# Kernel optimization log

Hardware: AMD Instinct MI355X
Metric: run time of the kernel (lower is better)

Reference implementation:

```python
import jax, jax.numpy as jnp
import numpy as np

B, T, H, W = 8, 16, 512, 512


def setup_inputs() -> dict:
    key = jax.random.key(0)
    k1, k2 = jax.random.split(key)
    img = jax.random.normal(k1, (B, H, W), dtype=jnp.float32)
    U = jax.random.normal(k2, (B, T, H, W, 2), dtype=jnp.float32)
    return {"img": img, "U": U}


def _warp(img, U):
    # img: (B,H,W), U: (B,T,H,W,2) displacement (di, dj). Output (B,T,H,W).
    b, h, w = img.shape
    ii = jnp.arange(h, dtype=jnp.float32)[:, None]   # (H,1)
    jj = jnp.arange(w, dtype=jnp.float32)[None, :]   # (1,W)
    si = ii - U[..., 0]                              # (B,T,H,W) sample rows
    sj = jj - U[..., 1]                              # (B,T,H,W) sample cols
    i0 = jnp.clip(jnp.floor(si).astype(jnp.int32), 0, h - 1)
    j0 = jnp.clip(jnp.floor(sj).astype(jnp.int32), 0, w - 1)
    i1 = jnp.clip(i0 + 1, 0, h - 1)
    j1 = jnp.clip(j0 + 1, 0, w - 1)
    # fractional weights computed AFTER clipping, matching the original
    di = si - i0.astype(jnp.float32)
    dj = sj - j0.astype(jnp.float32)

    def gather(im, ri, ci):  # im (H,W), ri/ci (T,H,W)
        return im[ri, ci]

    g = jax.vmap(gather)  # over batch
    f00 = g(img, i0, j0)
    f01 = g(img, i0, j1)
    f10 = g(img, i1, j0)
    f11 = g(img, i1, j1)
    f0 = f00 + (f01 - f00) * dj
    f1 = f10 + (f11 - f10) * dj
    return f0 + (f1 - f0) * di


def reference(img, U):
    return _warp(img, U)
```

## Files before the change

kernel.cpp:

```cpp
#include <hip/hip_runtime.h>

#define HH 512
#define WW 512
#define TT 16
#define NROWS 16
#define SLOT_OFF 7

typedef float vf4 __attribute__((ext_vector_type(4)));
typedef float vf2 __attribute__((ext_vector_type(2)));

__device__ __forceinline__ float warp_one(const float* __restrict__ lds,
                                          const float* __restrict__ im,
                                          int ic, float fi, float fj,
                                          float ux, float uy) {
    float si = fi - ux;
    float sj = fj - uy;
    int i0 = (int)floorf(si);
    int j0 = (int)floorf(sj);
    i0 = min(max(i0, 0), HH - 1);
    j0 = min(max(j0, 0), WW - 1);
    int i1 = min(i0 + 1, HH - 1);
    int j1 = min(j0 + 1, WW - 1);
    float di = si - (float)i0;
    float dj = sj - (float)j0;
    int s0 = i0 - ic + SLOT_OFF;
    int s1 = i1 - ic + SLOT_OFF;
    float f00, f01, f10, f11;
    if (((unsigned)s0 < NROWS) & ((unsigned)s1 < NROWS)) {
        f00 = lds[s0 * WW + j0];
        f01 = lds[s0 * WW + j1];
        f10 = lds[s1 * WW + j0];
        f11 = lds[s1 * WW + j1];
    } else {
        f00 = im[i0 * WW + j0];
        f01 = im[i0 * WW + j1];
        f10 = im[i1 * WW + j0];
        f11 = im[i1 * WW + j1];
    }
    float f0 = f00 + (f01 - f00) * dj;
    float f1 = f10 + (f11 - f10) * dj;
    return f0 + (f1 - f0) * di;
}

__global__ __launch_bounds__(256) void SpatialWarp_kernel(
    const float* __restrict__ img,
    const float* __restrict__ U,
    float* __restrict__ out)
{
    __shared__ float lds[NROWS * WW];

    int bid = blockIdx.x;
    int b = bid >> 9;
    int i = bid & (HH - 1);
    const float* im = img + (size_t)b * (HH * WW);

    int k = threadIdx.x;
    int j = k << 1;
    float fi = (float)i;
    float fj0 = (float)j, fj1 = (float)(j + 1);

    vf4 uu[TT];
#pragma unroll
    for (int t = 0; t < TT; ++t) {
        size_t rowoff = (((size_t)b * TT + t) * HH + i) * WW;
        uu[t] = __builtin_nontemporal_load(
            reinterpret_cast<const vf4*>(U + rowoff * 2) + k);
    }

    for (int idx = threadIdx.x; idx < NROWS * (WW / 4); idx += 256) {
        int s = idx >> 7;
        int c = idx & 127;
        int r = min(max(i - SLOT_OFF + s, 0), HH - 1);
        reinterpret_cast<vf4*>(lds)[idx] =
            reinterpret_cast<const vf4*>(im + (size_t)r * WW)[c];
    }
    __syncthreads();

#pragma unroll
    for (int t = 0; t < TT; ++t) {
        size_t rowoff = (((size_t)b * TT + t) * HH + i) * WW;
        vf4 u = uu[t];
        float r0 = warp_one(lds, im, i, fi, fj0, u.x, u.y);
        float r1 = warp_one(lds, im, i, fi, fj1, u.z, u.w);
        vf2 rv; rv.x = r0; rv.y = r1;
        __builtin_nontemporal_store(rv, reinterpret_cast<vf2*>(out + rowoff) + k);
    }
}

extern "C" void kernel_launch(void* const* d_in, const int* in_sizes, int n_in,
                              void* d_out, int out_size, void* d_ws, size_t ws_size,
                              hipStream_t stream) {
    const float* img = (const float*)d_in[0];
    const float* U   = (const float*)d_in[1];
    float* out = (float*)d_out;

    dim3 block(256);
    dim3 grid(8 * HH);
    hipLaunchKernelGGL(SpatialWarp_kernel, grid, block, 0, stream,
                       img, U, out);
}
```

Before: 88.37 us.

## Process two output rows per block sharing an LDS halo, prefetch U per step

Each block now handles two adjacent image rows and stages a 13-row LDS window (rows ip-5..ip+7), instead of a 16-row window per single row. This reduces redundant image-row loads into LDS per output row and halves the grid size. U is no longer loaded all 16 timesteps up front; it is software-prefetched one timestep ahead, cutting register pressure. The trade-off is a narrower halo around each row, so more samples may fall back to global-memory gathers, and fewer blocks are available for latency hiding.

```diff
diff --git a/kernel.cpp b/kernel.cpp
--- a/kernel.cpp
+++ b/kernel.cpp
@@ -3,15 +3,16 @@
 #define HH 512
 #define WW 512
 #define TT 16
-#define NROWS 16
-#define SLOT_OFF 7
+#define ROWS 2
+#define NR 13
+#define OFF 5
 
 typedef float vf4 __attribute__((ext_vector_type(4)));
 typedef float vf2 __attribute__((ext_vector_type(2)));
 
 __device__ __forceinline__ float warp_one(const float* __restrict__ lds,
                                           const float* __restrict__ im,
-                                          int ic, float fi, float fj,
+                                          int ip, float fi, float fj,
                                           float ux, float uy) {
     float si = fi - ux;
     float sj = fj - uy;
@@ -23,10 +24,10 @@
     int j1 = min(j0 + 1, WW - 1);
     float di = si - (float)i0;
     float dj = sj - (float)j0;
-    int s0 = i0 - ic + SLOT_OFF;
-    int s1 = i1 - ic + SLOT_OFF;
+    int s0 = i0 - ip + OFF;
+    int s1 = i1 - ip + OFF;
     float f00, f01, f10, f11;
-    if (((unsigned)s0 < NROWS) & ((unsigned)s1 < NROWS)) {
+    if (((unsigned)s0 < NR) & ((unsigned)s1 < NR)) {
         f00 = lds[s0 * WW + j0];
         f01 = lds[s0 * WW + j1];
         f10 = lds[s1 * WW + j0];
@@ -47,44 +48,56 @@
     const float* __restrict__ U,
     float* __restrict__ out)
 {
-    __shared__ float lds[NROWS * WW];
+    __shared__ float lds[NR * WW];
 
     int bid = blockIdx.x;
-    int b = bid >> 9;
-    int i = bid & (HH - 1);
+    int b  = bid >> 8;
+    int ip = (bid & 255) << 1;
     const float* im = img + (size_t)b * (HH * WW);
 
     int k = threadIdx.x;
     int j = k << 1;
-    float fi = (float)i;
     float fj0 = (float)j, fj1 = (float)(j + 1);
+    float fi0 = (float)ip, fi1 = (float)(ip + 1);
 
-    vf4 uu[TT];
-#pragma unroll
-    for (int t = 0; t < TT; ++t) {
-        size_t rowoff = (((size_t)b * TT + t) * HH + i) * WW;
-        uu[t] = __builtin_nontemporal_load(
-            reinterpret_cast<const vf4*>(U + rowoff * 2) + k);
-    }
+    size_t ubase = (((size_t)b * TT) * HH + ip) * (WW / 2);
+    const vf4* Uv = reinterpret_cast<const vf4*>(U);
 
-    for (int idx = threadIdx.x; idx < NROWS * (WW / 4); idx += 256) {
+    vf4 u0c = __builtin_nontemporal_load(Uv + ubase + k);
+    vf4 u1c = __builtin_nontemporal_load(Uv + ubase + (WW / 2) + k);
+
+    for (int idx = threadIdx.x; idx < NR * (WW / 4); idx += 256) {
         int s = idx >> 7;
         int c = idx & 127;
-        int r = min(max(i - SLOT_OFF + s, 0), HH - 1);
+        int r = min(max(ip - OFF + s, 0), HH - 1);
         reinterpret_cast<vf4*>(lds)[idx] =
             reinterpret_cast<const vf4*>(im + (size_t)r * WW)[c];
     }
     __syncthreads();
 
+    size_t ostride = (size_t)HH * WW;
 #pragma unroll
     for (int t = 0; t < TT; ++t) {
-        size_t rowoff = (((size_t)b * TT + t) * HH + i) * WW;
-        vf4 u = uu[t];
-        float r0 = warp_one(lds, im, i, fi, fj0, u.x, u.y);
-        float r1 = warp_one(lds, im, i, fi, fj1, u.z, u.w);
-        vf2 rv; rv.x = r0; rv.y = r1;
-        __builtin_nontemporal_store(rv, reinterpret_cast<vf2*>(out + rowoff) + k);
+        vf4 u0n, u1n;
+        if (t < TT - 1) {
+            size_t un = ubase + (size_t)(t + 1) * HH * (WW / 2);
+            u0n = __builtin_nontemporal_load(Uv + un + k);
+            u1n = __builtin_nontemporal_load(Uv + un + (WW / 2) + k);
+        }
+        float r00 = warp_one(lds, im, ip, fi0, fj0, u0c.x, u0c.y);
+        float r01 = warp_one(lds, im, ip, fi0, fj1, u0c.z, u0c.w);
+        float r10 = warp_one(lds, im, ip, fi1, fj0, u1c.x, u1c.y);
+        float r11 = warp_one(lds, im, ip, fi1, fj1, u1c.z, u1c.w);
+
+        size_t obase = (((size_t)b * TT + t) * HH + ip) * WW;
+        vf2 rv0; rv0.x = r00; rv0.y = r01;
+        vf2 rv1; rv1.x = r10; rv1.y = r11;
+        __builtin_nontemporal_store(rv0, reinterpret_cast<vf2*>(out + obase) + k);
+        __builtin_nontemporal_store(rv1, reinterpret_cast<vf2*>(out + obase + WW) + k);
+
+        u0c = u0n; u1c = u1n;
     }
+    (void)ostride;
 }
 
 extern "C" void kernel_launch(void* const* d_in, const int* in_sizes, int n_in,
@@ -95,7 +108,7 @@
     float* out = (float*)d_out;
 
     dim3 block(256);
-    dim3 grid(8 * HH);
+    dim3 grid(8 * (HH / ROWS));
     hipLaunchKernelGGL(SpatialWarp_kernel, grid, block, 0, stream,
                        img, U, out);
 }
```

After: 82.41 us. -6.7%, faster.
